# Optimization experiments

Measured on AMD Instinct MI355X. Metric: run time of the kernel, lower is better.

Reference implementation:

```python
import jax, jax.numpy as jnp
import numpy as np

N, FIN, H, O, K = 300000, 128, 64, 32, 5


def setup_inputs() -> dict:
    key = jax.random.key(0)
    ks = jax.random.split(key, 8)
    xav_uh = (2.0 / (FIN + H)) ** 0.5  # xavier_normal scale for Linear(FIN, H)
    xav_ho = (2.0 / (H + O)) ** 0.5
    return {
        "user": jax.random.normal(ks[0], (N, FIN), dtype=jnp.float32),
        "item": jax.random.normal(ks[1], (N, FIN), dtype=jnp.float32),
        "r": jax.random.randint(ks[2], (N,), 0, K),
        "c": jax.random.uniform(ks[3], (N,), dtype=jnp.float32),
        # relation-stacked Linear weights, torch layout [out, in] -> [K, H, FIN]
        "Wu": jax.random.normal(ks[4], (K, H, FIN), dtype=jnp.float32) * xav_uh,
        "bu": jnp.zeros((K, H), dtype=jnp.float32),
        "Wv": jax.random.normal(ks[5], (K, H, FIN), dtype=jnp.float32) * xav_uh,
        "bv": jnp.zeros((K, H), dtype=jnp.float32),
        "Wl": jax.random.normal(ks[6], (O, H), dtype=jnp.float32) * xav_ho,
        "bl": jnp.zeros((O,), dtype=jnp.float32),
    }


def reference(user, item, r, c, Wu, bu, Wv, bv, Wl, bl):
    # Per-row relation-indexed linear: out[i] = x[i] @ W[r[i]].T + b[r[i]]
    def rel_linear(x, W, b):
        allp = jnp.einsum("ni,khi->nkh", x, W) + b[None]  # [N, K, H]
        return jnp.take_along_axis(allp, r[:, None, None], axis=1)[:, 0, :]  # [N, H]

    u_next = c[:, None] * rel_linear(item, Wu, bu)  # messages from items to users
    v_next = c[:, None] * rel_linear(user, Wv, bv)  # messages from users to items
    u_out = jax.nn.relu(jax.nn.relu(u_next) @ Wl.T + bl)
    v_out = jax.nn.relu(jax.nn.relu(v_next) @ Wl.T + bl)
    return (u_out, v_out)
```

## Files before the change

### kernel.cpp

```cpp
#include <hip/hip_runtime.h>
#include <hip/hip_bf16.h>

#define N_ROWS 300000
#define FIN    128
#define HDIM   64
#define ODIM   32
#define KREL   5
#define BRT    128
#define NTT    ((N_ROWS + BRT - 1) / BRT)
#define TPB    4
#define NCHUNK ((NTT + TPB - 1) / TPB)

typedef __attribute__((ext_vector_type(8))) short bf8_t;
typedef __attribute__((ext_vector_type(4))) float f32x4;
typedef __attribute__((ext_vector_type(4))) unsigned int u32x4;

static __device__ __forceinline__ unsigned pk2(float lo, float hi) {
  __hip_bfloat162 h = __float22bfloat162_rn(make_float2(lo, hi));
  return *reinterpret_cast<unsigned*>(&h);
}

static __device__ __forceinline__ bf8_t cvt8(float4 a, float4 b) {
  u32x4 u;
  u.x = pk2(a.x, a.y);
  u.y = pk2(a.z, a.w);
  u.z = pk2(b.x, b.y);
  u.w = pk2(b.z, b.w);
  return __builtin_bit_cast(bf8_t, u);
}

static __device__ __forceinline__ void stbf4_pk(void* base, int byte, float4 v) {
  unsigned long long p = (unsigned long long)pk2(v.x, v.y)
                       | ((unsigned long long)pk2(v.z, v.w) << 32);
  *(unsigned long long*)((char*)base + byte) = p;
}

static __device__ __forceinline__ bf8_t lds_load16(const void* base, int byte) {
  return *(const bf8_t*)((const char*)base + byte);
}


__global__ __launch_bounds__(512, 1) void gcn_main(
    const float* __restrict__ user, const float* __restrict__ item,
    const int* __restrict__ r, const float* __restrict__ c,
    const float* __restrict__ Wu, const float* __restrict__ bu,
    const float* __restrict__ Wv, const float* __restrict__ bv,
    const float* __restrict__ Wl, const float* __restrict__ bl,
    float* __restrict__ out)
{
  __shared__ __align__(16) unsigned short sW[KREL * HDIM * FIN];
  __shared__ __align__(16) unsigned short sX[BRT * FIN];
  __shared__ float sB[KREL * HDIM];
  __shared__ int sSrc[TPB][BRT];
  __shared__ int sRel[TPB][BRT];
  __shared__ int sCnt[TPB][KREL];

  const int tid   = threadIdx.x;
  const int side  = blockIdx.x & 1;
  const int chunk = blockIdx.x >> 1;
  const int t_begin = chunk * TPB;
  if (t_begin >= NTT) return;
  const int t_end = (t_begin + TPB < NTT) ? t_begin + TPB : NTT;

  const float* X  = side ? user : item;
  const float* Wk = side ? Wv : Wu;
  const float* bk = side ? bv : bu;

  const int lane = tid & 63;
  const int wid  = tid >> 6;
  const int lrow = lane & 15;
  const int lkg  = lane >> 4;
  const int sh   = lane >> 5;
  const int c4   = lane & 31;

  {
    const int j = tid >> 7;
    const int i = tid & 127;
    int tj = (t_begin + j < NTT) ? t_begin + j : NTT - 1;
    int grow = tj * BRT + i;
    int rr = r[(grow < N_ROWS) ? grow : N_ROWS - 1];
    if (tid < TPB * KREL) sCnt[tid / KREL][tid % KREL] = 0;
    __syncthreads();
    int rank = atomicAdd(&sCnt[j][rr], 1);
    __syncthreads();
    if (tid < TPB) {
      int off = 0;
      #pragma unroll
      for (int k = 0; k < KREL; ++k) { int v = sCnt[tid][k]; sCnt[tid][k] = off; off += v; }
    }
    __syncthreads();
    int pos = sCnt[j][rr] + rank;
    sSrc[j][pos] = i;
    sRel[j][pos] = rr;
  }

  {
    const float4* w4 = (const float4*)Wk;
    #pragma unroll
    for (int j = 0; j < 20; ++j) {
      int f4   = j * 512 + tid;
      int k    = f4 >> 11;
      int rowk = (f4 >> 5) & 63;
      int cc   = f4 & 31;
      int byte = (k << 14) + ((rowk * 256 + cc * 8) ^ ((rowk & 7) << 4));
      stbf4_pk(sW, byte, w4[f4]);
    }
  }
  if (tid < KREL * HDIM) sB[tid] = bk[tid];

  bf8_t wl[2][2];
  #pragma unroll
  for (int n2 = 0; n2 < 2; ++n2)
    #pragma unroll
    for (int k2 = 0; k2 < 2; ++k2) {
      const float* p = Wl + (size_t)(n2 * 16 + lrow) * HDIM + k2 * 32 + lkg * 8;
      wl[n2][k2] = cvt8(*(const float4*)p, *(const float4*)(p + 4));
    }
  const float blv0 = bl[lrow];
  const float blv1 = bl[16 + lrow];

  char* myX = (char*)sX + wid * 4096;
  const int rowb_off = wid * 16;

  __syncthreads();

  #pragma unroll
  for (int it = 0; it < 8; ++it) {
    int slot = rowb_off + it * 2 + sh;
    int grow = t_begin * BRT + sSrc[0][slot];
    grow = (grow < N_ROWS) ? grow : N_ROWS - 1;
    float4 a = *(const float4*)(X + (size_t)grow * FIN + c4 * 4);
    int rl   = it * 2 + sh;
    int byte = (rl * 256 + c4 * 8) ^ ((rl & 7) << 4);
    stbf4_pk(myX, byte, a);
  }

  for (int t = t_begin; t < t_end; ++t) {
    const int j = t - t_begin;
    const int tile0 = t * BRT;
    const bool do_stage = (t + 1 < t_end);

    const int myrel = sRel[j][rowb_off + lrow];

    float4 ld[8];
    if (do_stage) {
      #pragma unroll
      for (int it = 0; it < 8; ++it) {
        int slot = rowb_off + it * 2 + sh;
        int grow = (t + 1) * BRT + sSrc[j + 1][slot];
        grow = (grow < N_ROWS) ? grow : N_ROWS - 1;
        ld[it] = *(const float4*)(X + (size_t)grow * FIN + c4 * 4);
      }
    }

    int lsrcQ[4], rQ[4]; float cQ[4];
    #pragma unroll
    for (int q = 0; q < 4; ++q) {
      int slot = rowb_off + lkg * 4 + q;
      int ls   = sSrc[j][slot];
      lsrcQ[q] = ls;
      rQ[q]    = sRel[j][slot];
      int rc   = tile0 + ls;
      cQ[q]    = c[(rc < N_ROWS) ? rc : N_ROWS - 1];
    }

    __builtin_amdgcn_sched_barrier(0);

    f32x4 acc[4];
    #pragma unroll
    for (int n = 0; n < 4; ++n) acc[n] = f32x4{0.f, 0.f, 0.f, 0.f};

    const bf8_t zero8 = {};
    const int axor = (lrow & 7) << 4;
    bf8_t au[4];
    #pragma unroll
    for (int kc = 0; kc < 4; ++kc) {
      const int kb = (kc * 32 + lkg * 8) * 2;
      au[kc] = lds_load16(myX, (lrow * 256 + kb) ^ axor);
    }
    #pragma unroll
    for (int k = 0; k < KREL; ++k) {
      if (__any(myrel == k)) {
        const int kofs = k << 14;
        #pragma unroll
        for (int kc = 0; kc < 4; ++kc) {
          const int kb = (kc * 32 + lkg * 8) * 2;
          bf8_t auk = (myrel == k) ? au[kc] : zero8;
          #pragma unroll
          for (int n = 0; n < 4; ++n) {
            int brow = n * 16 + lrow;
            int bx   = kofs + ((brow * 256 + kb) ^ ((brow & 7) << 4));
            acc[n] = __builtin_amdgcn_mfma_f32_16x16x32_bf16(auk, lds_load16(sW, bx), acc[n], 0, 0, 0);
          }
        }
      }
    }

    #pragma unroll
    for (int n = 0; n < 4; ++n) {
      int hcol = n * 16 + lrow;
      #pragma unroll
      for (int q = 0; q < 4; ++q) {
        int rr   = lkg * 4 + q;
        int byte = (rr * 128 + hcol * 2) ^ ((rr & 7) << 4);
        float bb = sB[rQ[q] * HDIM + hcol];
        float hv = fmaxf(cQ[q] * (acc[n][q] + bb), 0.f);
        *(unsigned short*)(myX + byte) = (unsigned short)(pk2(hv, hv) & 0xFFFFu);
      }
    }

    f32x4 acc2[2];
    acc2[0] = f32x4{0.f, 0.f, 0.f, 0.f};
    acc2[1] = f32x4{0.f, 0.f, 0.f, 0.f};
    #pragma unroll
    for (int k2 = 0; k2 < 2; ++k2) {
      const int kb = (k2 * 32 + lkg * 8) * 2;
      const int ax = (lrow * 128 + kb) ^ axor;
      bf8_t a2 = lds_load16(myX, ax);
      #pragma unroll
      for (int n2 = 0; n2 < 2; ++n2)
        acc2[n2] = __builtin_amdgcn_mfma_f32_16x16x32_bf16(a2, wl[n2][k2], acc2[n2], 0, 0, 0);
    }

    const size_t obase = (size_t)side * N_ROWS * ODIM;
    #pragma unroll
    for (int n2 = 0; n2 < 2; ++n2) {
      int col  = n2 * 16 + lrow;
      float bb = (n2 == 0) ? blv0 : blv1;
      #pragma unroll
      for (int q = 0; q < 4; ++q) {
        int row = tile0 + lsrcQ[q];
        if (row < N_ROWS)
          out[obase + (size_t)row * ODIM + col] = fmaxf(acc2[n2][q] + bb, 0.f);
      }
    }

    __builtin_amdgcn_sched_barrier(0);

    if (do_stage) {
      #pragma unroll
      for (int it = 0; it < 8; ++it) {
        int rl   = it * 2 + sh;
        int byte = (rl * 256 + c4 * 8) ^ ((rl & 7) << 4);
        stbf4_pk(myX, byte, ld[it]);
      }
    }
  }
}

extern "C" void kernel_launch(void* const* d_in, const int* in_sizes, int n_in,
                              void* d_out, int out_size, void* d_ws, size_t ws_size,
                              hipStream_t stream) {
  const float* user = (const float*)d_in[0];
  const float* item = (const float*)d_in[1];
  const int*   r    = (const int*)d_in[2];
  const float* c    = (const float*)d_in[3];
  const float* Wu   = (const float*)d_in[4];
  const float* bu   = (const float*)d_in[5];
  const float* Wv   = (const float*)d_in[6];
  const float* bv   = (const float*)d_in[7];
  const float* Wl   = (const float*)d_in[8];
  const float* bl   = (const float*)d_in[9];
  float* out = (float*)d_out;

  gcn_main<<<2 * NCHUNK, 512, 0, stream>>>(user, item, r, c, Wu, bu, Wv, bv,
                                           Wl, bl, out);
}
```

Baseline: 99.48 us.

## Pre-convert weights to bf16 in global memory and read B operands from cache

Adds a small pre-pass kernel that converts Wu and Wv to bf16 in the workspace. The main kernel no longer stages all relation weights into LDS each block (an 80KB LDS tile and a per-block conversion). Instead it reads MFMA B fragments directly from global/L2. With LDS shrunk, launch bounds allow two blocks per CU for more occupancy. The risk is per-MFMA global load latency and cache pressure in the inner loop, plus an extra kernel launch.

```diff
diff --git a/kernel.cpp b/kernel.cpp
--- a/kernel.cpp
+++ b/kernel.cpp
@@ -10,6 +10,7 @@
 #define NTT    ((N_ROWS + BRT - 1) / BRT)
 #define TPB    4
 #define NCHUNK ((NTT + TPB - 1) / TPB)
+#define WELEM  (KREL * HDIM * FIN)
 
 typedef __attribute__((ext_vector_type(8))) short bf8_t;
 typedef __attribute__((ext_vector_type(4))) float f32x4;
@@ -39,16 +40,27 @@
   return *(const bf8_t*)((const char*)base + byte);
 }
 
-
-__global__ __launch_bounds__(512, 1) void gcn_main(
+__global__ void wconv_kernel(const float* __restrict__ Wu, const float* __restrict__ Wv,
+                             unsigned long long* __restrict__ wubf,
+                             unsigned long long* __restrict__ wvbf) {
+  int i = blockIdx.x * 256 + threadIdx.x;
+  if (i < WELEM / 4) {
+    float4 a = ((const float4*)Wu)[i];
+    float4 b = ((const float4*)Wv)[i];
+    wubf[i] = (unsigned long long)pk2(a.x, a.y) | ((unsigned long long)pk2(a.z, a.w) << 32);
+    wvbf[i] = (unsigned long long)pk2(b.x, b.y) | ((unsigned long long)pk2(b.z, b.w) << 32);
+  }
+}
+
+
+__global__ __launch_bounds__(512, 2) void gcn_main(
     const float* __restrict__ user, const float* __restrict__ item,
     const int* __restrict__ r, const float* __restrict__ c,
-    const float* __restrict__ Wu, const float* __restrict__ bu,
-    const float* __restrict__ Wv, const float* __restrict__ bv,
+    const unsigned short* __restrict__ wubf, const unsigned short* __restrict__ wvbf,
+    const float* __restrict__ bu, const float* __restrict__ bv,
     const float* __restrict__ Wl, const float* __restrict__ bl,
     float* __restrict__ out)
 {
-  __shared__ __align__(16) unsigned short sW[KREL * HDIM * FIN];
   __shared__ __align__(16) unsigned short sX[BRT * FIN];
   __shared__ float sB[KREL * HDIM];
   __shared__ int sSrc[TPB][BRT];
@@ -62,8 +74,8 @@
   if (t_begin >= NTT) return;
   const int t_end = (t_begin + TPB < NTT) ? t_begin + TPB : NTT;
 
-  const float* X  = side ? user : item;
-  const float* Wk = side ? Wv : Wu;
+  const float* X = side ? user : item;
+  const unsigned short* Wg = side ? wvbf : wubf;
   const float* bk = side ? bv : bu;
 
   const int lane = tid & 63;
@@ -93,19 +105,6 @@
     sSrc[j][pos] = i;
     sRel[j][pos] = rr;
   }
-
-  {
-    const float4* w4 = (const float4*)Wk;
-    #pragma unroll
-    for (int j = 0; j < 20; ++j) {
-      int f4   = j * 512 + tid;
-      int k    = f4 >> 11;
-      int rowk = (f4 >> 5) & 63;
-      int cc   = f4 & 31;
-      int byte = (k << 14) + ((rowk * 256 + cc * 8) ^ ((rowk & 7) << 4));
-      stbf4_pk(sW, byte, w4[f4]);
-    }
-  }
   if (tid < KREL * HDIM) sB[tid] = bk[tid];
 
   bf8_t wl[2][2];
@@ -189,8 +188,8 @@
           #pragma unroll
           for (int n = 0; n < 4; ++n) {
             int brow = n * 16 + lrow;
-            int bx   = kofs + ((brow * 256 + kb) ^ ((brow & 7) << 4));
-            acc[n] = __builtin_amdgcn_mfma_f32_16x16x32_bf16(auk, lds_load16(sW, bx), acc[n], 0, 0, 0);
+            bf8_t w = *(const bf8_t*)((const char*)Wg + kofs + brow * 256 + kb);
+            acc[n] = __builtin_amdgcn_mfma_f32_16x16x32_bf16(auk, w, acc[n], 0, 0, 0);
           }
         }
       }
@@ -263,6 +262,11 @@
   const float* bl   = (const float*)d_in[9];
   float* out = (float*)d_out;
 
-  gcn_main<<<2 * NCHUNK, 512, 0, stream>>>(user, item, r, c, Wu, bu, Wv, bv,
-                                           Wl, bl, out);
-}
+  unsigned short* wubf = (unsigned short*)d_ws;
+  unsigned short* wvbf = wubf + WELEM;
+
+  wconv_kernel<<<(WELEM / 4 + 255) / 256, 256, 0, stream>>>(
+      Wu, Wv, (unsigned long long*)wubf, (unsigned long long*)wvbf);
+  gcn_main<<<2 * NCHUNK, 512, 0, stream>>>(user, item, r, c, wubf, wvbf,
+                                           bu, bv, Wl, bl, out);
+}
```

Measured after the change: 221.8 us. 2.23x slower.

## Pre-convert weights to swizzled bf16 once and DMA into LDS

Applied to the files above, without the earlier changes.

A small pre-kernel converts Wu/Wv to bf16 in the swizzled LDS layout and stores them in workspace. Each main block then copies its weight tile straight into LDS with global_load_lds, with no per-block fp32 load and conversion. This halves per-block weight traffic and removes conversion ALU work, and the weight copy can overlap with the relation sort. The cost is an extra kernel launch, plus no visible wait (vmcnt) before the LDS weights are used, so correctness depends on the later __syncthreads draining the loads.

```diff
diff --git a/kernel.cpp b/kernel.cpp
--- a/kernel.cpp
+++ b/kernel.cpp
@@ -10,6 +10,8 @@
 #define NTT    ((N_ROWS + BRT - 1) / BRT)
 #define TPB    4
 #define NCHUNK ((NTT + TPB - 1) / TPB)
+#define WELEM  (KREL * HDIM * FIN)
+#define WCHUNK (WELEM / 8)
 
 typedef __attribute__((ext_vector_type(8))) short bf8_t;
 typedef __attribute__((ext_vector_type(4))) float f32x4;
@@ -39,12 +41,35 @@
   return *(const bf8_t*)((const char*)base + byte);
 }
 
+__global__ void wconv_swz(const float* __restrict__ Wu, const float* __restrict__ Wv,
+                          u32x4* __restrict__ wus, u32x4* __restrict__ wvs) {
+  int i = blockIdx.x * 256 + threadIdx.x;
+  if (i < WCHUNK) {
+    int byte = i * 16;
+    int k    = byte >> 14;
+    int rem  = byte & 16383;
+    int rowk = rem >> 8;
+    int off  = rem & 255;
+    int soff = off ^ ((rowk & 7) << 4);
+    const float* pu = Wu + ((size_t)(k * 64 + rowk) * 128) + (soff >> 1);
+    const float* pv = Wv + ((size_t)(k * 64 + rowk) * 128) + (soff >> 1);
+    float4 a0 = *(const float4*)pu, a1 = *(const float4*)(pu + 4);
+    float4 b0 = *(const float4*)pv, b1 = *(const float4*)(pv + 4);
+    u32x4 ua; ua.x = pk2(a0.x, a0.y); ua.y = pk2(a0.z, a0.w);
+              ua.z = pk2(a1.x, a1.y); ua.w = pk2(a1.z, a1.w);
+    u32x4 ub; ub.x = pk2(b0.x, b0.y); ub.y = pk2(b0.z, b0.w);
+              ub.z = pk2(b1.x, b1.y); ub.w = pk2(b1.z, b1.w);
+    wus[i] = ua;
+    wvs[i] = ub;
+  }
+}
+
 
 __global__ __launch_bounds__(512, 1) void gcn_main(
     const float* __restrict__ user, const float* __restrict__ item,
     const int* __restrict__ r, const float* __restrict__ c,
-    const float* __restrict__ Wu, const float* __restrict__ bu,
-    const float* __restrict__ Wv, const float* __restrict__ bv,
+    const unsigned short* __restrict__ wus, const unsigned short* __restrict__ wvs,
+    const float* __restrict__ bu, const float* __restrict__ bv,
     const float* __restrict__ Wl, const float* __restrict__ bl,
     float* __restrict__ out)
 {
@@ -62,8 +87,8 @@
   if (t_begin >= NTT) return;
   const int t_end = (t_begin + TPB < NTT) ? t_begin + TPB : NTT;
 
-  const float* X  = side ? user : item;
-  const float* Wk = side ? Wv : Wu;
+  const float* X = side ? user : item;
+  const unsigned short* Wg = side ? wvs : wus;
   const float* bk = side ? bv : bu;
 
   const int lane = tid & 63;
@@ -72,6 +97,16 @@
   const int lkg  = lane >> 4;
   const int sh   = lane >> 5;
   const int c4   = lane & 31;
+
+  {
+    const char* src = (const char*)Wg + wid * 10240 + lane * 16;
+    char* dst = (char*)sW + wid * 10240;
+    #pragma unroll
+    for (int it = 0; it < 10; ++it)
+      __builtin_amdgcn_global_load_lds(
+          (const __attribute__((address_space(1))) void*)(src + it * 1024),
+          (__attribute__((address_space(3))) void*)(dst + it * 1024), 16, 0, 0);
+  }
 
   {
     const int j = tid >> 7;
@@ -92,19 +127,6 @@
     int pos = sCnt[j][rr] + rank;
     sSrc[j][pos] = i;
     sRel[j][pos] = rr;
-  }
-
-  {
-    const float4* w4 = (const float4*)Wk;
-    #pragma unroll
-    for (int j = 0; j < 20; ++j) {
-      int f4   = j * 512 + tid;
-      int k    = f4 >> 11;
-      int rowk = (f4 >> 5) & 63;
-      int cc   = f4 & 31;
-      int byte = (k << 14) + ((rowk * 256 + cc * 8) ^ ((rowk & 7) << 4));
-      stbf4_pk(sW, byte, w4[f4]);
-    }
   }
   if (tid < KREL * HDIM) sB[tid] = bk[tid];
 
@@ -263,6 +285,10 @@
   const float* bl   = (const float*)d_in[9];
   float* out = (float*)d_out;
 
-  gcn_main<<<2 * NCHUNK, 512, 0, stream>>>(user, item, r, c, Wu, bu, Wv, bv,
-                                           Wl, bl, out);
-}
+  unsigned short* wus = (unsigned short*)d_ws;
+  unsigned short* wvs = wus + WELEM;
+
+  wconv_swz<<<(WCHUNK + 255) / 256, 256, 0, stream>>>(Wu, Wv, (u32x4*)wus, (u32x4*)wvs);
+  gcn_main<<<2 * NCHUNK, 512, 0, stream>>>(user, item, r, c, wus, wvs,
+                                           bu, bv, Wl, bl, out);
+}
```

Measured after the change: 102.1 us. 2.7% more time.

## Load input rows directly into MFMA register layout, bypass LDS staging

Applied to the files above, without the earlier changes.

Each lane now loads the exact float4s of its row that it needs as the MFMA A operand and converts them to bf16 in registers. This removes the coalesced-load, LDS store and LDS reload round trip for the X tile and shrinks the shared buffer to hold only the hidden activations. The per-lane global reads are now strided 32-byte pieces across rows, which coalesces less well, and the prefetch double buffer lives in registers. It also adds s_setprio around the MFMA loops and drops a sched_barrier.

```diff
diff --git a/kernel.cpp b/kernel.cpp
--- a/kernel.cpp
+++ b/kernel.cpp
@@ -49,7 +49,7 @@
     float* __restrict__ out)
 {
   __shared__ __align__(16) unsigned short sW[KREL * HDIM * FIN];
-  __shared__ __align__(16) unsigned short sX[BRT * FIN];
+  __shared__ __align__(16) unsigned short sH[8 * 1024];
   __shared__ float sB[KREL * HDIM];
   __shared__ int sSrc[TPB][BRT];
   __shared__ int sRel[TPB][BRT];
@@ -70,8 +70,6 @@
   const int wid  = tid >> 6;
   const int lrow = lane & 15;
   const int lkg  = lane >> 4;
-  const int sh   = lane >> 5;
-  const int c4   = lane & 31;
 
   {
     const int j = tid >> 7;
@@ -119,20 +117,21 @@
   const float blv0 = bl[lrow];
   const float blv1 = bl[16 + lrow];
 
-  char* myX = (char*)sX + wid * 4096;
+  char* myH = (char*)sH + wid * 2048;
   const int rowb_off = wid * 16;
 
   __syncthreads();
 
-  #pragma unroll
-  for (int it = 0; it < 8; ++it) {
-    int slot = rowb_off + it * 2 + sh;
-    int grow = t_begin * BRT + sSrc[0][slot];
+  float4 ldA[8];
+  {
+    int grow = t_begin * BRT + sSrc[0][rowb_off + lrow];
     grow = (grow < N_ROWS) ? grow : N_ROWS - 1;
-    float4 a = *(const float4*)(X + (size_t)grow * FIN + c4 * 4);
-    int rl   = it * 2 + sh;
-    int byte = (rl * 256 + c4 * 8) ^ ((rl & 7) << 4);
-    stbf4_pk(myX, byte, a);
+    const float* prow = X + (size_t)grow * FIN + lkg * 8;
+    #pragma unroll
+    for (int kc = 0; kc < 4; ++kc) {
+      ldA[2 * kc]     = *(const float4*)(prow + kc * 32);
+      ldA[2 * kc + 1] = *(const float4*)(prow + kc * 32 + 4);
+    }
   }
 
   for (int t = t_begin; t < t_end; ++t) {
@@ -142,14 +141,15 @@
 
     const int myrel = sRel[j][rowb_off + lrow];
 
-    float4 ld[8];
+    float4 ldB[8];
     if (do_stage) {
-      #pragma unroll
-      for (int it = 0; it < 8; ++it) {
-        int slot = rowb_off + it * 2 + sh;
-        int grow = (t + 1) * BRT + sSrc[j + 1][slot];
-        grow = (grow < N_ROWS) ? grow : N_ROWS - 1;
-        ld[it] = *(const float4*)(X + (size_t)grow * FIN + c4 * 4);
+      int grow = (t + 1) * BRT + sSrc[j + 1][rowb_off + lrow];
+      grow = (grow < N_ROWS) ? grow : N_ROWS - 1;
+      const float* prow = X + (size_t)grow * FIN + lkg * 8;
+      #pragma unroll
+      for (int kc = 0; kc < 4; ++kc) {
+        ldB[2 * kc]     = *(const float4*)(prow + kc * 32);
+        ldB[2 * kc + 1] = *(const float4*)(prow + kc * 32 + 4);
       }
     }
 
@@ -174,14 +174,14 @@
     const int axor = (lrow & 7) << 4;
     bf8_t au[4];
     #pragma unroll
-    for (int kc = 0; kc < 4; ++kc) {
-      const int kb = (kc * 32 + lkg * 8) * 2;
-      au[kc] = lds_load16(myX, (lrow * 256 + kb) ^ axor);
-    }
+    for (int kc = 0; kc < 4; ++kc)
+      au[kc] = cvt8(*(float4*)&ldA[2 * kc], *(float4*)&ldA[2 * kc + 1]);
+
     #pragma unroll
     for (int k = 0; k < KREL; ++k) {
       if (__any(myrel == k)) {
         const int kofs = k << 14;
+        __builtin_amdgcn_s_setprio(1);
         #pragma unroll
         for (int kc = 0; kc < 4; ++kc) {
           const int kb = (kc * 32 + lkg * 8) * 2;
@@ -193,6 +193,7 @@
             acc[n] = __builtin_amdgcn_mfma_f32_16x16x32_bf16(auk, lds_load16(sW, bx), acc[n], 0, 0, 0);
           }
         }
+        __builtin_amdgcn_s_setprio(0);
       }
     }
 
@@ -205,22 +206,24 @@
         int byte = (rr * 128 + hcol * 2) ^ ((rr & 7) << 4);
         float bb = sB[rQ[q] * HDIM + hcol];
         float hv = fmaxf(cQ[q] * (acc[n][q] + bb), 0.f);
-        *(unsigned short*)(myX + byte) = (unsigned short)(pk2(hv, hv) & 0xFFFFu);
+        *(unsigned short*)(myH + byte) = (unsigned short)(pk2(hv, hv) & 0xFFFFu);
       }
     }
 
     f32x4 acc2[2];
     acc2[0] = f32x4{0.f, 0.f, 0.f, 0.f};
     acc2[1] = f32x4{0.f, 0.f, 0.f, 0.f};
+    __builtin_amdgcn_s_setprio(1);
     #pragma unroll
     for (int k2 = 0; k2 < 2; ++k2) {
       const int kb = (k2 * 32 + lkg * 8) * 2;
       const int ax = (lrow * 128 + kb) ^ axor;
-      bf8_t a2 = lds_load16(myX, ax);
+      bf8_t a2 = lds_load16(myH, ax);
       #pragma unroll
       for (int n2 = 0; n2 < 2; ++n2)
         acc2[n2] = __builtin_amdgcn_mfma_f32_16x16x32_bf16(a2, wl[n2][k2], acc2[n2], 0, 0, 0);
     }
+    __builtin_amdgcn_s_setprio(0);
 
     const size_t obase = (size_t)side * N_ROWS * ODIM;
     #pragma unroll
@@ -235,15 +238,9 @@
       }
     }
 
-    __builtin_amdgcn_sched_barrier(0);
-
     if (do_stage) {
       #pragma unroll
-      for (int it = 0; it < 8; ++it) {
-        int rl   = it * 2 + sh;
-        int byte = (rl * 256 + c4 * 8) ^ ((rl & 7) << 4);
-        stbf4_pk(myX, byte, ld[it]);
-      }
+      for (int i = 0; i < 8; ++i) ldA[i] = ldB[i];
     }
   }
 }
```

Result: slower. 110.5 us (+11.1%).
